# Kernel tuning notes

Measured on AMD Instinct MI355X. Metric: run time of the kernel, lower is better.

The kernel has to match this reference:

```python
import jax, jax.numpy as jnp
import numpy as np


def _diag_perm(h, w):
    # Matches torch loop: offsets -(h-1)..w-1, within offset ordered by row i.
    ii, jj = np.meshgrid(np.arange(h), np.arange(w), indexing='ij')
    idx = np.lexsort((ii.ravel(), (jj - ii).ravel())).astype(np.int32)
    inv = np.argsort(idx).astype(np.int32)
    return jnp.asarray(idx), jnp.asarray(inv)


def _mamba(tok, ln_g, ln_b, Win, conv_w, conv_b, Wx, Wdt, bdt, A_log, Dp, Wout):
    # tok: (B, L, C). MambaLayer = LayerNorm + standard Mamba block.
    di, dc = conv_w.shape
    ds = A_log.shape[-1]
    dtr = Wdt.shape[-1]
    mu = tok.mean(-1, keepdims=True)
    var = ((tok - mu) ** 2).mean(-1, keepdims=True)
    t = (tok - mu) * jax.lax.rsqrt(var + 1e-5) * ln_g + ln_b
    xz = jnp.einsum('blc,ec->ble', t, Win)          # (B,L,2*di)
    xh, z = jnp.split(xz, 2, axis=-1)
    # causal depthwise conv over sequence
    xc = jnp.transpose(xh, (0, 2, 1))               # (B,di,L)
    xc = jax.lax.conv_general_dilated(
        xc, conv_w[:, None, :], (1,), [(dc - 1, 0)],
        dimension_numbers=('NCH', 'OIH', 'NCH'), feature_group_count=di)
    u = jax.nn.silu(jnp.transpose(xc, (0, 2, 1)) + conv_b)  # (B,L,di)
    proj = jnp.einsum('bld,ed->ble', u, Wx)
    dt_r, Bm, Cm = jnp.split(proj, [dtr, dtr + ds], axis=-1)
    dt = jax.nn.softplus(jnp.einsum('blr,dr->bld', dt_r, Wdt) + bdt)  # (B,L,di)
    A = -jnp.exp(A_log)                              # (di,ds)

    def step(h, inp):
        dt_t, B_t, C_t, u_t = inp                    # (B,di) (B,ds) (B,ds) (B,di)
        dA = jnp.exp(dt_t[..., None] * A)            # (B,di,ds)
        h = dA * h + dt_t[..., None] * B_t[:, None, :] * u_t[..., None]
        y = jnp.einsum('bds,bs->bd', h, C_t)
        return h, y

    h0 = jnp.zeros((u.shape[0], di, ds), u.dtype)
    _, ys = jax.lax.scan(step, h0, (jnp.moveaxis(dt, 1, 0), jnp.moveaxis(Bm, 1, 0),
                                    jnp.moveaxis(Cm, 1, 0), jnp.moveaxis(u, 1, 0)))
    y = jnp.moveaxis(ys, 0, 1) + u * Dp              # (B,L,di)
    y = y * jax.nn.silu(z)
    return jnp.einsum('bld,cd->blc', y, Wout)


def _forward(x, ln_g, ln_b, Win, conv_w, conv_b, Wx, Wdt, bdt, A_log, Dp, Wout):
    b, c, h, w = x.shape
    idx, inv = _diag_perm(h, w)

    def mam(d, tok):
        return _mamba(tok, ln_g[d], ln_b[d], Win[d], conv_w[d], conv_b[d],
                      Wx[d], Wdt[d], bdt[d], A_log[d], Dp[d], Wout[d])

    row_tok = x.reshape(b, c, h * w).transpose(0, 2, 1)
    row_feat = mam(0, row_tok).transpose(0, 2, 1).reshape(b, c, h, w)
    col_tok = x.transpose(0, 1, 3, 2).reshape(b, c, w * h).transpose(0, 2, 1)
    col_feat = mam(1, col_tok).transpose(0, 2, 1).reshape(b, c, w, h).transpose(0, 1, 3, 2)
    diag_feat = mam(2, row_tok[:, idx, :])[:, inv, :].transpose(0, 2, 1).reshape(b, c, h, w)
    xf = x[:, :, :, ::-1]
    anti_tok = xf.reshape(b, c, h * w).transpose(0, 2, 1)[:, idx, :]
    anti_feat = mam(3, anti_tok)[:, inv, :].transpose(0, 2, 1).reshape(b, c, h, w)[:, :, :, ::-1]
    gate = jax.nn.sigmoid((row_feat + col_feat + diag_feat + anti_feat) / 4.0)
    return x * gate


def setup_inputs() -> dict:
    key = jax.random.key(0)
    ks = jax.random.split(key, 8)
    B, C, H, W = 4, 96, 48, 48
    DI, DS, DC, DTR = 192, 16, 4, 6
    s = 0.05
    return {
        'x': jax.random.normal(ks[0], (B, C, H, W), jnp.float32),
        'ln_g': jnp.ones((4, C), jnp.float32),
        'ln_b': jnp.zeros((4, C), jnp.float32),
        'Win': jax.random.normal(ks[1], (4, 2 * DI, C), jnp.float32) * s,
        'conv_w': jax.random.normal(ks[2], (4, DI, DC), jnp.float32) * s,
        'conv_b': jnp.zeros((4, DI), jnp.float32),
        'Wx': jax.random.normal(ks[3], (4, DTR + 2 * DS, DI), jnp.float32) * s,
        'Wdt': jax.random.normal(ks[4], (4, DI, DTR), jnp.float32) * s,
        'bdt': jax.random.normal(ks[5], (4, DI), jnp.float32) * s,
        'A_log': jnp.log(jnp.broadcast_to(jnp.arange(1, DS + 1, dtype=jnp.float32), (4, DI, DS))),
        'Dp': jnp.ones((4, DI), jnp.float32),
        'Wout': jax.random.normal(ks[6], (4, C, DI), jnp.float32) * s,
    }


def reference(x, ln_g, ln_b, Win, conv_w, conv_b, Wx, Wdt, bdt, A_log, Dp, Wout):
    return _forward(x, ln_g, ln_b, Win, conv_w, conv_b, Wx, Wdt, bdt, A_log, Dp, Wout)
```

## Files before the change

### kernel.cpp

```cpp
#include <hip/hip_runtime.h>
#include <math.h>

#define LSEQ 2304
#define LC 32
#define NCH 72

typedef unsigned short u16;
typedef unsigned int u32;
typedef __attribute__((ext_vector_type(8))) short bf16x8;
typedef __attribute__((ext_vector_type(4))) float f32x4;

__device__ __forceinline__ float sigmoidf_(float v){ return 1.f/(1.f+__expf(-v)); }
__device__ __forceinline__ u16 f2b(float f){
  union{float f; u32 u;} v; v.f = f;
  u32 r = v.u + 0x7fffu + ((v.u >> 16) & 1u);
  return (u16)(r >> 16);
}
__device__ __forceinline__ float b2f(u16 h){
  union{u32 u; float f;} v; v.u = ((u32)h) << 16; return v.f;
}
__device__ __forceinline__ u16 f2h(float f){
  _Float16 h = (_Float16)f;
  union{_Float16 h; u16 u;} v; v.h = h; return v.u;
}
__device__ __forceinline__ float h2f(u16 u){
  union{u16 u; _Float16 h;} v; v.u = u; return (float)v.h;
}
__device__ __forceinline__ uint2 pack4(float a, float b, float c, float d){
  uint2 o;
  o.x = (u32)f2b(a) | ((u32)f2b(b) << 16);
  o.y = (u32)f2b(c) | ((u32)f2b(d) << 16);
  return o;
}
__device__ __forceinline__ float softplus_(float v){
  return fmaxf(v, 0.f) + __logf(1.f + __expf(-fabsf(v)));
}

__global__ void g_kernel(int* __restrict__ g, int* __restrict__ flag){
  int tid = threadIdx.x;
  if (tid == 0) *flag = 1;
  for (int l = tid; l < LSEQ; l += 256){
    g[l] = l;
    g[LSEQ + l] = (l % 48) * 48 + l / 48;
  }
  for (int p = tid; p < LSEQ; p += 256){
    int i = p / 48, j = p % 48, dd = j - i;
    int off = (dd <= 0) ? (47 + dd) * (48 + dd) / 2
                        : 1176 + 48 * (dd - 1) - dd * (dd - 1) / 2;
    int l = off + min(i, j);
    g[2 * LSEQ + l] = p;
  }
  __syncthreads();
  for (int l = tid; l < LSEQ; l += 256){
    int p2 = g[2 * LSEQ + l];
    g[3 * LSEQ + l] = (p2 / 48) * 48 + 47 - (p2 % 48);
  }
}

__global__ void prep_fold(const float* __restrict__ Win, const float* __restrict__ ln_g,
                          const float* __restrict__ ln_b, const float* __restrict__ A_log,
                          const float* __restrict__ Wout, const float* __restrict__ Wx,
                          const float* __restrict__ Wdt, const float* __restrict__ bdt,
                          u16* __restrict__ WinMF, float* __restrict__ b2,
                          float* __restrict__ Aneg2, u16* __restrict__ WoutMF,
                          u16* __restrict__ Wcomb, float* __restrict__ bcomb,
                          int* __restrict__ flag){
  int i = blockIdx.x * 256 + threadIdx.x;
  if (i < 4*192*16){
    float a = -expf(A_log[i]);
    Aneg2[i] = a * 1.44269504f;
    int s = i & 15;
    float a0 = -expf(A_log[i - s]);
    if (fabsf(a - (float)(s + 1) * a0) > 1e-5f * fabsf(a) + 1e-30f)
      atomicAnd(flag, 0);
  }
  if (i < 4*384*96){
    int d = i / 36864, r = i % 36864, c = r % 96;
    WinMF[i] = f2b(Win[i] * ln_g[d*96 + c]);
  }
  if (i < 4*96*192) WoutMF[i] = f2b(Wout[i]);
  if (i < 4*224*192){
    int d = i / 43008, r = i % 43008, e = r / 192, c = r % 192;
    float w;
    if (e < 192){
      const float* wdt = &Wdt[(size_t)(d*192 + e) * 6];
      w = 0.f;
      #pragma unroll
      for (int r6 = 0; r6 < 6; ++r6) w += wdt[r6] * Wx[(size_t)(d*38 + r6) * 192 + c];
    } else if (e < 208){
      w = Wx[(size_t)(d*38 + 6 + (e - 192)) * 192 + c];
    } else {
      w = Wx[(size_t)(d*38 + 22 + (e - 208)) * 192 + c];
    }
    Wcomb[i] = f2b(w);
  }
  if (i < 4*224){
    int d = i / 224, e = i % 224;
    bcomb[i] = (e < 192) ? bdt[d*192 + e] : 0.f;
  }
  if (i < 4*384){
    int d = i / 384;
    const float* wr = &Win[(size_t)i * 96];
    const float* lb = &ln_b[d * 96];
    float s = 0.f;
    for (int c = 0; c < 96; ++c) s += wr[c] * lb[c];
    b2[i] = s;
  }
}

__global__ __launch_bounds__(256) void ln_kernel(const float* __restrict__ x, u16* __restrict__ n){
  int t = blockIdx.x * 256 + threadIdx.x;
  if (t >= 4 * 2304) return;
  int b = t / 2304, p = t % 2304;
  const float* xp = x + (size_t)b * 96 * 2304 + p;
  float s = 0.f;
  for (int c = 0; c < 96; ++c) s += xp[c * 2304];
  float mu = s * (1.f / 96.f);
  float v = 0.f;
  for (int c = 0; c < 96; ++c){ float dv = xp[c * 2304] - mu; v += dv * dv; }
  float rs = rsqrtf(v * (1.f / 96.f) + 1e-5f);
  u16* np_ = n + (size_t)t * 96;
  for (int c = 0; c < 96; ++c) np_[c] = f2b((xp[c * 2304] - mu) * rs);
}

__global__ __launch_bounds__(256) void kproj(const u16* __restrict__ nbf,
    const u16* __restrict__ WinMF, const float* __restrict__ b2,
    u16* __restrict__ xz){
  int d = blockIdx.y;
  int wv = threadIdx.x >> 6, lane = threadIdx.x & 63;
  int lr = lane & 15, lg = lane >> 4;
  int r0 = blockIdx.x * 64 + wv * 16;
  const u16* Ap = nbf + (size_t)(r0 + lr) * 96 + lg * 8;
  bf16x8 tk0 = *(const bf16x8*)(Ap);
  bf16x8 tk1 = *(const bf16x8*)(Ap + 32);
  bf16x8 tk2 = *(const bf16x8*)(Ap + 64);
  const u16* Wb = WinMF + (size_t)d * 36864 + (size_t)lr * 96 + lg * 8;
  const float* b2d = b2 + d * 384;
  u16* out = xz + ((size_t)d * 9216 + r0 + lr) * 384;
  for (int grp = 0; grp < 3; ++grp){
    f32x4 acc[8];
    #pragma unroll
    for (int t = 0; t < 8; ++t)
      acc[t] = *(const f32x4*)&b2d[(grp*8 + t)*16 + lg*4];
    #pragma unroll
    for (int t = 0; t < 8; ++t){
      const u16* wp = Wb + (size_t)(grp*8 + t) * 1536;
      acc[t] = __builtin_amdgcn_mfma_f32_16x16x32_bf16(*(const bf16x8*)(wp     ), tk0, acc[t], 0, 0, 0);
      acc[t] = __builtin_amdgcn_mfma_f32_16x16x32_bf16(*(const bf16x8*)(wp + 32), tk1, acc[t], 0, 0, 0);
      acc[t] = __builtin_amdgcn_mfma_f32_16x16x32_bf16(*(const bf16x8*)(wp + 64), tk2, acc[t], 0, 0, 0);
    }
    #pragma unroll
    for (int t = 0; t < 8; ++t){
      uint2 o = pack4(acc[t][0], acc[t][1], acc[t][2], acc[t][3]);
      *(uint2*)&out[(grp*8 + t)*16 + lg*4] = o;
    }
  }
}

__global__ __launch_bounds__(256) void kconv(const u16* __restrict__ xz, const int* __restrict__ g,
    const float* __restrict__ conv_w, const float* __restrict__ conv_b,
    u16* __restrict__ u, u16* __restrict__ sz){
  __shared__ u16 xh[67][200];
  int d = blockIdx.z, b = blockIdx.y, l0 = blockIdx.x * 64;
  int tid = threadIdx.x;
  const int* gd = g + d * LSEQ;
  const u16* xzd = xz + (size_t)d * 9216 * 384 + (size_t)b * LSEQ * 384;
  for (int i = tid; i < 67*24; i += 256){
    int lt = i / 24, j = i % 24;
    int gl = l0 - 3 + lt;
    uint4 v = make_uint4(0u, 0u, 0u, 0u);
    if (gl >= 0){
      int p = gd[gl];
      v = *(const uint4*)(xzd + (size_t)p * 384 + j * 8);
    }
    *(uint4*)&xh[lt][j*8] = v;
  }
  size_t obase = ((size_t)(d*4 + b) * LSEQ + l0) * 192;
  for (int i = tid; i < 64*48; i += 256){
    int lt = i / 48, j = (i % 48) * 4;
    int p = gd[l0 + lt];
    uint2 zv = *(const uint2*)(xzd + (size_t)p * 384 + 192 + j);
    float z0 = b2f((u16)(zv.x & 0xffff)), z1 = b2f((u16)(zv.x >> 16));
    float z2 = b2f((u16)(zv.y & 0xffff)), z3 = b2f((u16)(zv.y >> 16));
    z0 *= sigmoidf_(z0); z1 *= sigmoidf_(z1); z2 *= sigmoidf_(z2); z3 *= sigmoidf_(z3);
    *(uint2*)(sz + obase + (size_t)lt * 192 + j) = pack4(z0, z1, z2, z3);
  }
  __syncthreads();
  for (int i = tid; i < 64*48; i += 256){
    int lt = i / 48, j = (i % 48) * 4;
    float a0 = conv_b[d*192 + j + 0];
    float a1 = conv_b[d*192 + j + 1];
    float a2 = conv_b[d*192 + j + 2];
    float a3 = conv_b[d*192 + j + 3];
    const float4 w0 = *(const float4*)&conv_w[(size_t)(d*192 + j + 0) * 4];
    const float4 w1 = *(const float4*)&conv_w[(size_t)(d*192 + j + 1) * 4];
    const float4 w2 = *(const float4*)&conv_w[(size_t)(d*192 + j + 2) * 4];
    const float4 w3 = *(const float4*)&conv_w[(size_t)(d*192 + j + 3) * 4];
    const float* w0p = (const float*)&w0;
    const float* w1p = (const float*)&w1;
    const float* w2p = (const float*)&w2;
    const float* w3p = (const float*)&w3;
    #pragma unroll
    for (int kk = 0; kk < 4; ++kk){
      uint2 xv = *(const uint2*)&xh[lt + kk][j];
      a0 += w0p[kk] * b2f((u16)(xv.x & 0xffff));
      a1 += w1p[kk] * b2f((u16)(xv.x >> 16));
      a2 += w2p[kk] * b2f((u16)(xv.y & 0xffff));
      a3 += w3p[kk] * b2f((u16)(xv.y >> 16));
    }
    a0 *= sigmoidf_(a0); a1 *= sigmoidf_(a1); a2 *= sigmoidf_(a2); a3 *= sigmoidf_(a3);
    *(uint2*)(u + obase + (size_t)lt * 192 + j) = pack4(a0, a1, a2, a3);
  }
}

__global__ __launch_bounds__(256) void kernBM(const u16* __restrict__ u,
    const u16* __restrict__ Wcomb, const float* __restrict__ bcomb,
    u16* __restrict__ dtb, float* __restrict__ Bm, float* __restrict__ Cm){
  __shared__ u16 ush[64 * 200];
  int d = blockIdx.y;
  int tid = threadIdx.x;
  int tile0 = blockIdx.x * 64;
  const u16* ub = u + ((size_t)d * 4 * LSEQ + tile0) * 192;
  for (int i = tid; i < 64*24; i += 256){
    int row = i / 24, c8 = i % 24;
    *(uint4*)&ush[row*200 + c8*8] = *(const uint4*)&ub[(size_t)row*192 + c8*8];
  }
  __syncthreads();
  int wv = tid >> 6, lane = tid & 63;
  int lr = lane & 15, lg = lane >> 4;
  const u16* urow = &ush[(wv*16 + lr)*200 + lg*8];
  bf16x8 tk[6];
  #pragma unroll
  for (int kc = 0; kc < 6; ++kc) tk[kc] = *(const bf16x8*)(urow + kc*32);
  const u16* Wb = Wcomb + (size_t)d * 224 * 192 + (size_t)lr * 192 + lg * 8;
  bf16x8 bw[2][6];
  #pragma unroll
  for (int kc = 0; kc < 6; ++kc) bw[0][kc] = *(const bf16x8*)(Wb + kc*32);
  size_t tokrow = (size_t)d * 4 * LSEQ + tile0 + wv*16 + lr;
  for (int t = 0; t < 14; ++t){
    int cur = t & 1;
    if (t < 13){
      const u16* wp = Wb + (size_t)(t + 1) * 3072;
      #pragma unroll
      for (int kc = 0; kc < 6; ++kc) bw[cur^1][kc] = *(const bf16x8*)(wp + kc*32);
    }
    f32x4 a = (f32x4){0.f, 0.f, 0.f, 0.f};
    #pragma unroll
    for (int kc = 0; kc < 6; ++kc)
      a = __builtin_amdgcn_mfma_f32_16x16x32_bf16(bw[cur][kc], tk[kc], a, 0, 0, 0);
    if (t < 12){
      f32x4 bb = *(const f32x4*)&bcomb[d*224 + t*16 + lg*4];
      float s0 = softplus_(a[0] + bb[0]);
      float s1 = softplus_(a[1] + bb[1]);
      float s2 = softplus_(a[2] + bb[2]);
      float s3 = softplus_(a[3] + bb[3]);
      uint2 o;
      o.x = (u32)f2h(s0) | ((u32)f2h(s1) << 16);
      o.y = (u32)f2h(s2) | ((u32)f2h(s3) << 16);
      *(uint2*)&dtb[tokrow * 192 + t*16 + lg*4] = o;
    } else if (t == 12){
      *(float4*)&Bm[tokrow * 16 + lg*4] = make_float4(a[0], a[1], a[2], a[3]);
    } else {
      *(float4*)&Cm[tokrow * 16 + lg*4] = make_float4(a[0], a[1], a[2], a[3]);
    }
  }
}

__global__ __launch_bounds__(192) void kernC1(const u16* __restrict__ dtb, const u16* __restrict__ u,
    const float* __restrict__ Bm, const float* __restrict__ Aneg2, const int* __restrict__ flag,
    u16* __restrict__ hfin, float* __restrict__ Send){
  __shared__ float Bsh[LC*16];
  int ch = blockIdx.x, b = blockIdx.y, d = blockIdx.z;
  int seq = d*4 + b;
  int di = threadIdx.x;
  size_t tb = (size_t)seq * LSEQ + ch * LC;
  const float* bp = Bm + tb * 16;
  for (int i = di; i < LC*16; i += 192) Bsh[i] = bp[i];
  const u16* dtp = dtb + tb * 192;
  const u16* up  = u   + tb * 192;
  float h[16];
  #pragma unroll
  for (int s = 0; s < 16; ++s) h[s] = 0.f;
  float Sacc = 0.f;
  __syncthreads();
  if (*flag){
    float A2_0 = Aneg2[(d*192 + di) * 16];
    for (int j = 0; j < LC; ++j){
      float dtv = h2f(dtp[j*192 + di]);
      float uv  = b2f(up[j*192 + di]);
      float Bs[16];
      {
        const float4* b4 = (const float4*)&Bsh[j * 16];
        #pragma unroll
        for (int q = 0; q < 4; ++q){ float4 v = b4[q]; Bs[q*4]=v.x; Bs[q*4+1]=v.y; Bs[q*4+2]=v.z; Bs[q*4+3]=v.w; }
      }
      float dtu = dtv * uv;
      float e1 = __builtin_amdgcn_exp2f(dtv * A2_0);
      float e2 = e1*e1, e4 = e2*e2, e8 = e4*e4;
      float p[8];
      p[0]=e1; p[1]=e2; p[2]=e1*e2; p[3]=e4; p[4]=e1*e4; p[5]=e2*e4; p[6]=p[2]*e4; p[7]=e8;
      #pragma unroll
      for (int s = 0; s < 8; ++s){
        h[s] = p[s]*h[s] + dtu*Bs[s];
        float q = p[s]*e8;
        h[s+8] = q*h[s+8] + dtu*Bs[s+8];
      }
      Sacc += dtv;
    }
  } else {
    float A2[16];
    {
      const float4* ap = (const float4*)&Aneg2[(d*192 + di) * 16];
      #pragma unroll
      for (int q = 0; q < 4; ++q){ float4 a4 = ap[q]; A2[q*4]=a4.x; A2[q*4+1]=a4.y; A2[q*4+2]=a4.z; A2[q*4+3]=a4.w; }
    }
    for (int j = 0; j < LC; ++j){
      float dtv = h2f(dtp[j*192 + di]);
      float uv  = b2f(up[j*192 + di]);
      float Bs[16];
      {
        const float4* b4 = (const float4*)&Bsh[j * 16];
        #pragma unroll
        for (int q = 0; q < 4; ++q){ float4 v = b4[q]; Bs[q*4]=v.x; Bs[q*4+1]=v.y; Bs[q*4+2]=v.z; Bs[q*4+3]=v.w; }
      }
      float dtu = dtv * uv;
      #pragma unroll
      for (int s = 0; s < 16; ++s)
        h[s] = __builtin_amdgcn_exp2f(dtv * A2[s]) * h[s] + dtu * Bs[s];
      Sacc += dtv;
    }
  }
  u16* hf = &hfin[((size_t)seq * NCH + ch) * 3072 + di * 16];
  uint4 o0, o1;
  o0.x = (u32)f2b(h[0])  | ((u32)f2b(h[1])  << 16);
  o0.y = (u32)f2b(h[2])  | ((u32)f2b(h[3])  << 16);
  o0.z = (u32)f2b(h[4])  | ((u32)f2b(h[5])  << 16);
  o0.w = (u32)f2b(h[6])  | ((u32)f2b(h[7])  << 16);
  o1.x = (u32)f2b(h[8])  | ((u32)f2b(h[9])  << 16);
  o1.y = (u32)f2b(h[10]) | ((u32)f2b(h[11]) << 16);
  o1.z = (u32)f2b(h[12]) | ((u32)f2b(h[13]) << 16);
  o1.w = (u32)f2b(h[14]) | ((u32)f2b(h[15]) << 16);
  *(uint4*)hf = o0;
  *(uint4*)(hf + 8) = o1;
  Send[((size_t)seq * NCH + ch) * 192 + di] = Sacc;
}

__global__ __launch_bounds__(256) void kernC2(const u16* __restrict__ hfin, const float* __restrict__ Send,
    const float* __restrict__ Aneg2, u16* __restrict__ hin){
  int t = blockIdx.x * 256 + threadIdx.x;
  int seq = t / 3072, q = t % 3072;
  int di = q >> 4, s = q & 15;
  int d = seq >> 2;
  float A2 = Aneg2[(d*192 + di)*16 + s];
  float hr = 0.f;
  const u16* hf = hfin + (size_t)seq * NCH * 3072 + q;
  u16* hi = hin + (size_t)seq * NCH * 3072 + q;
  const float* Se = Send + (size_t)seq * NCH * 192 + di;
  for (int ch = 0; ch < NCH; ++ch){
    hi[(size_t)ch * 3072] = f2b(hr);
    hr = b2f(hf[(size_t)ch * 3072]) + __builtin_amdgcn_exp2f(A2 * Se[(size_t)ch * 192]) * hr;
  }
}

__global__ __launch_bounds__(192) void kernC3(const u16* __restrict__ dtb, const u16* __restrict__ u,
    const float* __restrict__ Bm, const float* __restrict__ Cm,
    const float* __restrict__ Aneg2, const int* __restrict__ flag, const u16* __restrict__ hin,
    const u16* __restrict__ sz, const float* __restrict__ Dp,
    u16* __restrict__ val){
  __shared__ float Bsh[LC*16];
  __shared__ float Csh[LC*16];
  int ch = blockIdx.x, b = blockIdx.y, d = blockIdx.z;
  int seq = d*4 + b;
  int di = threadIdx.x;
  size_t tb = (size_t)seq * LSEQ + ch * LC;
  const float* bp = Bm + tb * 16;
  const float* cp = Cm + tb * 16;
  for (int i = di; i < LC*16; i += 192){ Bsh[i] = bp[i]; Csh[i] = cp[i]; }
  float h[16];
  {
    const uint4* hi4 = (const uint4*)&hin[((size_t)seq * NCH + ch) * 3072 + di * 16];
    uint4 v0 = hi4[0], v1 = hi4[1];
    h[0]=b2f((u16)(v0.x&0xffff)); h[1]=b2f((u16)(v0.x>>16));
    h[2]=b2f((u16)(v0.y&0xffff)); h[3]=b2f((u16)(v0.y>>16));
    h[4]=b2f((u16)(v0.z&0xffff)); h[5]=b2f((u16)(v0.z>>16));
    h[6]=b2f((u16)(v0.w&0xffff)); h[7]=b2f((u16)(v0.w>>16));
    h[8]=b2f((u16)(v1.x&0xffff)); h[9]=b2f((u16)(v1.x>>16));
    h[10]=b2f((u16)(v1.y&0xffff)); h[11]=b2f((u16)(v1.y>>16));
    h[12]=b2f((u16)(v1.z&0xffff)); h[13]=b2f((u16)(v1.z>>16));
    h[14]=b2f((u16)(v1.w&0xffff)); h[15]=b2f((u16)(v1.w>>16));
  }
  float Dpv = Dp[d*192 + di];
  const u16* dtp = dtb + tb * 192;
  const u16* up  = u   + tb * 192;
  const u16* szp = sz  + tb * 192;
  u16* vp = val + tb * 192;
  __syncthreads();
  if (*flag){
    float A2_0 = Aneg2[(d*192 + di) * 16];
    for (int j = 0; j < LC; ++j){
      float dtv = h2f(dtp[j*192 + di]);
      float uv  = b2f(up[j*192 + di]);
      float Bs[16], Cs[16];
      {
        const float4* b4 = (const float4*)&Bsh[j * 16];
        const float4* c4 = (const float4*)&Csh[j * 16];
        #pragma unroll
        for (int q = 0; q < 4; ++q){
          float4 v = b4[q]; Bs[q*4]=v.x; Bs[q*4+1]=v.y; Bs[q*4+2]=v.z; Bs[q*4+3]=v.w;
          float4 w = c4[q]; Cs[q*4]=w.x; Cs[q*4+1]=w.y; Cs[q*4+2]=w.z; Cs[q*4+3]=w.w;
        }
      }
      float dtu = dtv * uv;
      float e1 = __builtin_amdgcn_exp2f(dtv * A2_0);
      float e2 = e1*e1, e4 = e2*e2, e8 = e4*e4;
      float p[8];
      p[0]=e1; p[1]=e2; p[2]=e1*e2; p[3]=e4; p[4]=e1*e4; p[5]=e2*e4; p[6]=p[2]*e4; p[7]=e8;
      float yv = 0.f;
      #pragma unroll
      for (int s = 0; s < 8; ++s){
        h[s] = p[s]*h[s] + dtu*Bs[s];
        yv += h[s]*Cs[s];
        float q = p[s]*e8;
        h[s+8] = q*h[s+8] + dtu*Bs[s+8];
        yv += h[s+8]*Cs[s+8];
      }
      float szv = b2f(szp[j*192 + di]);
      vp[j*192 + di] = f2b((yv + uv * Dpv) * szv);
    }
  } else {
    float A2[16];
    {
      const float4* ap = (const float4*)&Aneg2[(d*192 + di) * 16];
      #pragma unroll
      for (int q = 0; q < 4; ++q){ float4 a4 = ap[q]; A2[q*4]=a4.x; A2[q*4+1]=a4.y; A2[q*4+2]=a4.z; A2[q*4+3]=a4.w; }
    }
    for (int j = 0; j < LC; ++j){
      float dtv = h2f(dtp[j*192 + di]);
      float uv  = b2f(up[j*192 + di]);
      float Bs[16], Cs[16];
      {
        const float4* b4 = (const float4*)&Bsh[j * 16];
        const float4* c4 = (const float4*)&Csh[j * 16];
        #pragma unroll
        for (int q = 0; q < 4; ++q){
          float4 v = b4[q]; Bs[q*4]=v.x; Bs[q*4+1]=v.y; Bs[q*4+2]=v.z; Bs[q*4+3]=v.w;
          float4 w = c4[q]; Cs[q*4]=w.x; Cs[q*4+1]=w.y; Cs[q*4+2]=w.z; Cs[q*4+3]=w.w;
        }
      }
      float dtu = dtv * uv;
      float yv = 0.f;
      #pragma unroll
      for (int s = 0; s < 16; ++s){
        h[s] = __builtin_amdgcn_exp2f(dtv * A2[s]) * h[s] + dtu * Bs[s];
        yv += h[s] * Cs[s];
      }
      float szv = b2f(szp[j*192 + di]);
      vp[j*192 + di] = f2b((yv + uv * Dpv) * szv);
    }
  }
}

__global__ __launch_bounds__(256) void kout(const u16* __restrict__ val,
    const u16* __restrict__ WoutMF, const int* __restrict__ g,
    u16* __restrict__ feat){
  int d = blockIdx.z, b = blockIdx.y;
  int wv = threadIdx.x >> 6, lane = threadIdx.x & 63;
  int lr = lane & 15, lg = lane >> 4;
  int l0 = blockIdx.x * 64 + wv * 16;
  const u16* Ap = val + ((size_t)(d*4 + b) * LSEQ + l0 + lr) * 192 + lg * 8;
  bf16x8 tk[6];
  #pragma unroll
  for (int kc = 0; kc < 6; ++kc) tk[kc] = *(const bf16x8*)(Ap + kc*32);
  const u16* Wb = WoutMF + (size_t)d * 18432 + (size_t)lr * 192 + lg * 8;
  f32x4 acc[6];
  #pragma unroll
  for (int t = 0; t < 6; ++t) acc[t] = (f32x4){0.f, 0.f, 0.f, 0.f};
  #pragma unroll
  for (int t = 0; t < 6; ++t){
    const u16* wp = Wb + (size_t)t * 3072;
    #pragma unroll
    for (int kc = 0; kc < 6; ++kc)
      acc[t] = __builtin_amdgcn_mfma_f32_16x16x32_bf16(*(const bf16x8*)(wp + kc*32), tk[kc], acc[t], 0, 0, 0);
  }
  u16* fd = feat + (size_t)(d*4 + b) * LSEQ * 96;
  int p = g[d*LSEQ + l0 + lr];
  #pragma unroll
  for (int t = 0; t < 6; ++t){
    uint2 o = pack4(acc[t][0], acc[t][1], acc[t][2], acc[t][3]);
    *(uint2*)&fd[(size_t)p * 96 + t*16 + lg*4] = o;
  }
}

__global__ __launch_bounds__(256) void kernE(const float* __restrict__ x, const u16* __restrict__ feat,
    float* __restrict__ out){
  __shared__ float acc[64 * 97];
  int p0 = blockIdx.x * 64, b = blockIdx.y;
  int tid = threadIdx.x;
  const size_t DS_ = (size_t)4 * LSEQ * 96;
  size_t base = ((size_t)b * LSEQ + p0) * 96;
  for (int i = tid; i < 3072; i += 256){
    int pp = i / 48, c2 = (i % 48) * 2;
    size_t o = base + (size_t)pp * 96 + c2;
    u32 v0 = *(const u32*)(feat + o);
    u32 v1 = *(const u32*)(feat + DS_ + o);
    u32 v2 = *(const u32*)(feat + 2*DS_ + o);
    u32 v3 = *(const u32*)(feat + 3*DS_ + o);
    float s0 = b2f((u16)(v0 & 0xffff)) + b2f((u16)(v1 & 0xffff)) + b2f((u16)(v2 & 0xffff)) + b2f((u16)(v3 & 0xffff));
    float s1 = b2f((u16)(v0 >> 16)) + b2f((u16)(v1 >> 16)) + b2f((u16)(v2 >> 16)) + b2f((u16)(v3 >> 16));
    acc[pp*97 + c2] = s0;
    acc[pp*97 + c2 + 1] = s1;
  }
  __syncthreads();
  for (int i = tid; i < 6144; i += 256){
    int c = i / 64, pp = i % 64;
    size_t o = ((size_t)b * 96 + c) * LSEQ + p0 + pp;
    out[o] = x[o] * sigmoidf_(acc[pp*97 + c] * 0.25f);
  }
}

extern "C" void kernel_launch(void* const* d_in, const int* in_sizes, int n_in,
                              void* d_out, int out_size, void* d_ws, size_t ws_size,
                              hipStream_t stream) {
  const float* x      = (const float*)d_in[0];
  const float* ln_g   = (const float*)d_in[1];
  const float* ln_b   = (const float*)d_in[2];
  const float* Win    = (const float*)d_in[3];
  const float* conv_w = (const float*)d_in[4];
  const float* conv_b = (const float*)d_in[5];
  const float* Wx     = (const float*)d_in[6];
  const float* Wdt    = (const float*)d_in[7];
  const float* bdt    = (const float*)d_in[8];
  const float* A_log  = (const float*)d_in[9];
  const float* Dp     = (const float*)d_in[10];
  const float* Wout   = (const float*)d_in[11];

  char* W = (char*)d_ws;
  char* W0 = W;
  auto alloc = [&](size_t bytes) -> char* {
    char* p = W; W += (bytes + 255) & ~(size_t)255; return p;
  };
  int*   g      = (int*)  alloc((size_t)4 * LSEQ * 4);
  int*   flag   = (int*)  alloc(256);
  float* Aneg2  = (float*)alloc((size_t)4 * 192 * 16 * 4);
  float* b2     = (float*)alloc((size_t)4 * 384 * 4);
  u16*   WinMF  = (u16*)  alloc((size_t)4 * 384 * 96 * 2);
  u16*   WoutMF = (u16*)  alloc((size_t)4 * 96 * 192 * 2);
  u16*   Wcomb  = (u16*)  alloc((size_t)4 * 224 * 192 * 2);
  float* bcomb  = (float*)alloc((size_t)4 * 224 * 4);
  u16*   nbf    = (u16*)  alloc((size_t)9216 * 96 * 2);
  u16*   xz     = (u16*)  alloc((size_t)4 * 9216 * 384 * 2);
  u16*   ubf    = (u16*)  alloc((size_t)16 * LSEQ * 192 * 2);
  u16*   szbf   = (u16*)  alloc((size_t)16 * LSEQ * 192 * 2);
  u16*   dtb    = (u16*)  alloc((size_t)16 * LSEQ * 192 * 2);
  float* Bm     = (float*)alloc((size_t)16 * LSEQ * 16 * 4);
  float* Cm     = (float*)alloc((size_t)16 * LSEQ * 16 * 4);
  u16*   valbf  = (u16*)  alloc((size_t)16 * LSEQ * 192 * 2);
  float* Send   = (float*)alloc((size_t)16 * NCH * 192 * 4);
  u16*   hfin   = (u16*)  alloc((size_t)16 * NCH * 3072 * 2);
  u16*   hin    = (u16*)  alloc((size_t)16 * NCH * 3072 * 2);
  u16*   feat   = (u16*)  alloc((size_t)16 * LSEQ * 96 * 2);
  if ((size_t)(W - W0) > ws_size) return;

  g_kernel<<<1, 256, 0, stream>>>(g, flag);
  prep_fold<<<768, 256, 0, stream>>>(Win, ln_g, ln_b, A_log, Wout, Wx, Wdt, bdt,
                                     WinMF, b2, Aneg2, WoutMF, Wcomb, bcomb, flag);
  ln_kernel<<<36, 256, 0, stream>>>(x, nbf);
  kproj<<<dim3(144, 4), 256, 0, stream>>>(nbf, WinMF, b2, xz);
  kconv<<<dim3(36, 4, 4), 256, 0, stream>>>(xz, g, conv_w, conv_b, ubf, szbf);
  kernBM<<<dim3(144, 4), 256, 0, stream>>>(ubf, Wcomb, bcomb, dtb, Bm, Cm);
  kernC1<<<dim3(NCH, 4, 4), 192, 0, stream>>>(dtb, ubf, Bm, Aneg2, flag, hfin, Send);
  kernC2<<<192, 256, 0, stream>>>(hfin, Send, Aneg2, hin);
  kernC3<<<dim3(NCH, 4, 4), 192, 0, stream>>>(dtb, ubf, Bm, Cm, Aneg2, flag, hin, szbf, Dp, valbf);
  kout<<<dim3(36, 4, 4), 256, 0, stream>>>(valbf, WoutMF, g, feat);
  kernE<<<dim3(36, 4), 256, 0, stream>>>(x, feat, (float*)d_out);
}
```

Before: 203.4 us.

## Fuse input projection into conv, scan into out-projection, parallelize LayerNorm

The input projection is now computed inside the conv kernel from gathered normalized tokens staged in shared memory, which removes the large xz intermediate buffer and one launch. The final scan kernel now keeps its outputs in shared memory and applies the Wout MFMA projection directly, which removes the val buffer and the separate kout kernel. LayerNorm splits channels across four threads per position, reduces through shared memory, and writes vectorized stores. The trade-offs are that the projection recomputes 16 halo rows per tile, the fused blocks use more shared memory, and the variance is now computed in one pass as E[x^2]-mu^2.

```diff
diff --git a/kernel.cpp b/kernel.cpp
--- a/kernel.cpp
+++ b/kernel.cpp
@@ -109,83 +109,90 @@
 }
 
 __global__ __launch_bounds__(256) void ln_kernel(const float* __restrict__ x, u16* __restrict__ n){
-  int t = blockIdx.x * 256 + threadIdx.x;
-  if (t >= 4 * 2304) return;
-  int b = t / 2304, p = t % 2304;
+  __shared__ float red[512];
+  int tid = threadIdx.x;
+  int s = tid & 63, q = tid >> 6;
+  int T = blockIdx.x * 64 + s;
+  int b = T / 2304, p = T % 2304;
   const float* xp = x + (size_t)b * 96 * 2304 + p;
-  float s = 0.f;
-  for (int c = 0; c < 96; ++c) s += xp[c * 2304];
-  float mu = s * (1.f / 96.f);
-  float v = 0.f;
-  for (int c = 0; c < 96; ++c){ float dv = xp[c * 2304] - mu; v += dv * dv; }
-  float rs = rsqrtf(v * (1.f / 96.f) + 1e-5f);
-  u16* np_ = n + (size_t)t * 96;
-  for (int c = 0; c < 96; ++c) np_[c] = f2b((xp[c * 2304] - mu) * rs);
-}
-
-__global__ __launch_bounds__(256) void kproj(const u16* __restrict__ nbf,
-    const u16* __restrict__ WinMF, const float* __restrict__ b2,
-    u16* __restrict__ xz){
-  int d = blockIdx.y;
-  int wv = threadIdx.x >> 6, lane = threadIdx.x & 63;
-  int lr = lane & 15, lg = lane >> 4;
-  int r0 = blockIdx.x * 64 + wv * 16;
-  const u16* Ap = nbf + (size_t)(r0 + lr) * 96 + lg * 8;
-  bf16x8 tk0 = *(const bf16x8*)(Ap);
-  bf16x8 tk1 = *(const bf16x8*)(Ap + 32);
-  bf16x8 tk2 = *(const bf16x8*)(Ap + 64);
-  const u16* Wb = WinMF + (size_t)d * 36864 + (size_t)lr * 96 + lg * 8;
-  const float* b2d = b2 + d * 384;
-  u16* out = xz + ((size_t)d * 9216 + r0 + lr) * 384;
-  for (int grp = 0; grp < 3; ++grp){
-    f32x4 acc[8];
-    #pragma unroll
-    for (int t = 0; t < 8; ++t)
-      acc[t] = *(const f32x4*)&b2d[(grp*8 + t)*16 + lg*4];
-    #pragma unroll
-    for (int t = 0; t < 8; ++t){
-      const u16* wp = Wb + (size_t)(grp*8 + t) * 1536;
-      acc[t] = __builtin_amdgcn_mfma_f32_16x16x32_bf16(*(const bf16x8*)(wp     ), tk0, acc[t], 0, 0, 0);
-      acc[t] = __builtin_amdgcn_mfma_f32_16x16x32_bf16(*(const bf16x8*)(wp + 32), tk1, acc[t], 0, 0, 0);
-      acc[t] = __builtin_amdgcn_mfma_f32_16x16x32_bf16(*(const bf16x8*)(wp + 64), tk2, acc[t], 0, 0, 0);
-    }
-    #pragma unroll
-    for (int t = 0; t < 8; ++t){
-      uint2 o = pack4(acc[t][0], acc[t][1], acc[t][2], acc[t][3]);
-      *(uint2*)&out[(grp*8 + t)*16 + lg*4] = o;
-    }
-  }
-}
-
-__global__ __launch_bounds__(256) void kconv(const u16* __restrict__ xz, const int* __restrict__ g,
+  float vals[24];
+  float sum = 0.f, ss = 0.f;
+  #pragma unroll
+  for (int k = 0; k < 24; ++k){
+    float v = xp[(size_t)(q*24 + k) * 2304];
+    vals[k] = v; sum += v; ss += v*v;
+  }
+  red[q*64 + s] = sum;
+  red[256 + q*64 + s] = ss;
+  __syncthreads();
+  float S = red[s] + red[64+s] + red[128+s] + red[192+s];
+  float Q = red[256+s] + red[320+s] + red[384+s] + red[448+s];
+  float mu = S * (1.f/96.f);
+  float var = Q * (1.f/96.f) - mu*mu;
+  float rs = rsqrtf(var + 1e-5f);
+  u32 w[12];
+  #pragma unroll
+  for (int k = 0; k < 12; ++k){
+    float v0 = (vals[2*k]   - mu) * rs;
+    float v1 = (vals[2*k+1] - mu) * rs;
+    w[k] = (u32)f2b(v0) | ((u32)f2b(v1) << 16);
+  }
+  uint4* np_ = (uint4*)(n + (size_t)T * 96 + q*24);
+  np_[0] = make_uint4(w[0], w[1], w[2],  w[3]);
+  np_[1] = make_uint4(w[4], w[5], w[6],  w[7]);
+  np_[2] = make_uint4(w[8], w[9], w[10], w[11]);
+}
+
+__global__ __launch_bounds__(256) void kprojconv(const u16* __restrict__ nbf,
+    const int* __restrict__ g, const u16* __restrict__ WinMF, const float* __restrict__ b2,
     const float* __restrict__ conv_w, const float* __restrict__ conv_b,
     u16* __restrict__ u, u16* __restrict__ sz){
-  __shared__ u16 xh[67][200];
+  __shared__ u16 tl[80][200];
+  __shared__ u16 xh[80][200];
   int d = blockIdx.z, b = blockIdx.y, l0 = blockIdx.x * 64;
   int tid = threadIdx.x;
+  int seq = d*4 + b;
   const int* gd = g + d * LSEQ;
-  const u16* xzd = xz + (size_t)d * 9216 * 384 + (size_t)b * LSEQ * 384;
-  for (int i = tid; i < 67*24; i += 256){
-    int lt = i / 24, j = i % 24;
+  for (int i = tid; i < 67*12; i += 256){
+    int lt = i / 12, j = i % 12;
     int gl = l0 - 3 + lt;
     uint4 v = make_uint4(0u, 0u, 0u, 0u);
     if (gl >= 0){
       int p = gd[gl];
-      v = *(const uint4*)(xzd + (size_t)p * 384 + j * 8);
-    }
-    *(uint4*)&xh[lt][j*8] = v;
-  }
-  size_t obase = ((size_t)(d*4 + b) * LSEQ + l0) * 192;
-  for (int i = tid; i < 64*48; i += 256){
-    int lt = i / 48, j = (i % 48) * 4;
-    int p = gd[l0 + lt];
-    uint2 zv = *(const uint2*)(xzd + (size_t)p * 384 + 192 + j);
-    float z0 = b2f((u16)(zv.x & 0xffff)), z1 = b2f((u16)(zv.x >> 16));
-    float z2 = b2f((u16)(zv.y & 0xffff)), z3 = b2f((u16)(zv.y >> 16));
-    z0 *= sigmoidf_(z0); z1 *= sigmoidf_(z1); z2 *= sigmoidf_(z2); z3 *= sigmoidf_(z3);
-    *(uint2*)(sz + obase + (size_t)lt * 192 + j) = pack4(z0, z1, z2, z3);
-  }
-  __syncthreads();
+      v = *(const uint4*)(nbf + (size_t)(b*2304 + p) * 96 + j*8);
+    }
+    *(uint4*)&tl[lt][j*8] = v;
+  }
+  __syncthreads();
+  int wv = tid >> 6, lane = tid & 63;
+  int lr = lane & 15, lg = lane >> 4;
+  const u16* Wb = WinMF + (size_t)d * 36864 + (size_t)lr * 96 + lg * 8;
+  const float* b2d = b2 + d * 384;
+  size_t zbase = (size_t)seq * LSEQ * 192;
+  for (int rt = wv; rt < 5; rt += 4){
+    int row = rt*16 + lr;
+    bf16x8 tk0 = *(const bf16x8*)&tl[row][      lg*8];
+    bf16x8 tk1 = *(const bf16x8*)&tl[row][32  + lg*8];
+    bf16x8 tk2 = *(const bf16x8*)&tl[row][64  + lg*8];
+    bool valid = (l0 + row >= 3);
+    for (int te = 0; te < 24; ++te){
+      const u16* wp = Wb + (size_t)te * 1536;
+      f32x4 acc = *(const f32x4*)&b2d[te*16 + lg*4];
+      acc = __builtin_amdgcn_mfma_f32_16x16x32_bf16(*(const bf16x8*)(wp     ), tk0, acc, 0, 0, 0);
+      acc = __builtin_amdgcn_mfma_f32_16x16x32_bf16(*(const bf16x8*)(wp + 32), tk1, acc, 0, 0, 0);
+      acc = __builtin_amdgcn_mfma_f32_16x16x32_bf16(*(const bf16x8*)(wp + 64), tk2, acc, 0, 0, 0);
+      if (te < 12){
+        uint2 o = valid ? pack4(acc[0], acc[1], acc[2], acc[3]) : make_uint2(0u, 0u);
+        *(uint2*)&xh[row][te*16 + lg*4] = o;
+      } else if (row >= 3 && row < 67){
+        float z0 = acc[0], z1 = acc[1], z2 = acc[2], z3 = acc[3];
+        z0 *= sigmoidf_(z0); z1 *= sigmoidf_(z1); z2 *= sigmoidf_(z2); z3 *= sigmoidf_(z3);
+        *(uint2*)(sz + zbase + (size_t)(l0 + row - 3) * 192 + (te-12)*16 + lg*4) = pack4(z0, z1, z2, z3);
+      }
+    }
+  }
+  __syncthreads();
+  size_t obase = ((size_t)seq * LSEQ + l0) * 192;
   for (int i = tid; i < 64*48; i += 256){
     int lt = i / 48, j = (i % 48) * 4;
     float a0 = conv_b[d*192 + j + 0];
@@ -362,20 +369,26 @@
   }
 }
 
-__global__ __launch_bounds__(192) void kernC3(const u16* __restrict__ dtb, const u16* __restrict__ u,
+__global__ __launch_bounds__(384) void kscan2out(const u16* __restrict__ dtb, const u16* __restrict__ u,
     const float* __restrict__ Bm, const float* __restrict__ Cm,
     const float* __restrict__ Aneg2, const int* __restrict__ flag, const u16* __restrict__ hin,
     const u16* __restrict__ sz, const float* __restrict__ Dp,
-    u16* __restrict__ val){
-  __shared__ float Bsh[LC*16];
-  __shared__ float Csh[LC*16];
-  int ch = blockIdx.x, b = blockIdx.y, d = blockIdx.z;
+    const u16* __restrict__ WoutMF, const int* __restrict__ g,
+    u16* __restrict__ feat){
+  __shared__ float Bsh[64*16];
+  __shared__ float Csh[64*16];
+  __shared__ u16 vsh[64][200];
+  int b = blockIdx.y, d = blockIdx.z;
   int seq = d*4 + b;
-  int di = threadIdx.x;
-  size_t tb = (size_t)seq * LSEQ + ch * LC;
-  const float* bp = Bm + tb * 16;
-  const float* cp = Cm + tb * 16;
-  for (int i = di; i < LC*16; i += 192){ Bsh[i] = bp[i]; Csh[i] = cp[i]; }
+  int l0 = blockIdx.x * 64;
+  int tid = threadIdx.x;
+  int gc = tid / 192, di = tid % 192;
+  int ch = blockIdx.x * 2 + gc;
+  {
+    const float* bp = Bm + ((size_t)seq * LSEQ + l0) * 16;
+    const float* cp = Cm + ((size_t)seq * LSEQ + l0) * 16;
+    for (int i = tid; i < 64*16; i += 384){ Bsh[i] = bp[i]; Csh[i] = cp[i]; }
+  }
   float h[16];
   {
     const uint4* hi4 = (const uint4*)&hin[((size_t)seq * NCH + ch) * 3072 + di * 16];
@@ -390,10 +403,10 @@
     h[14]=b2f((u16)(v1.w&0xffff)); h[15]=b2f((u16)(v1.w>>16));
   }
   float Dpv = Dp[d*192 + di];
+  size_t tb = (size_t)seq * LSEQ + ch * LC;
   const u16* dtp = dtb + tb * 192;
   const u16* up  = u   + tb * 192;
   const u16* szp = sz  + tb * 192;
-  u16* vp = val + tb * 192;
   __syncthreads();
   if (*flag){
     float A2_0 = Aneg2[(d*192 + di) * 16];
@@ -402,8 +415,8 @@
       float uv  = b2f(up[j*192 + di]);
       float Bs[16], Cs[16];
       {
-        const float4* b4 = (const float4*)&Bsh[j * 16];
-        const float4* c4 = (const float4*)&Csh[j * 16];
+        const float4* b4 = (const float4*)&Bsh[(gc*32 + j) * 16];
+        const float4* c4 = (const float4*)&Csh[(gc*32 + j) * 16];
         #pragma unroll
         for (int q = 0; q < 4; ++q){
           float4 v = b4[q]; Bs[q*4]=v.x; Bs[q*4+1]=v.y; Bs[q*4+2]=v.z; Bs[q*4+3]=v.w;
@@ -425,7 +438,7 @@
         yv += h[s+8]*Cs[s+8];
       }
       float szv = b2f(szp[j*192 + di]);
-      vp[j*192 + di] = f2b((yv + uv * Dpv) * szv);
+      vsh[gc*32 + j][di] = f2b((yv + uv * Dpv) * szv);
     }
   } else {
     float A2[16];
@@ -439,8 +452,8 @@
       float uv  = b2f(up[j*192 + di]);
       float Bs[16], Cs[16];
       {
-        const float4* b4 = (const float4*)&Bsh[j * 16];
-        const float4* c4 = (const float4*)&Csh[j * 16];
+        const float4* b4 = (const float4*)&Bsh[(gc*32 + j) * 16];
+        const float4* c4 = (const float4*)&Csh[(gc*32 + j) * 16];
         #pragma unroll
         for (int q = 0; q < 4; ++q){
           float4 v = b4[q]; Bs[q*4]=v.x; Bs[q*4+1]=v.y; Bs[q*4+2]=v.z; Bs[q*4+3]=v.w;
@@ -455,39 +468,35 @@
         yv += h[s] * Cs[s];
       }
       float szv = b2f(szp[j*192 + di]);
-      vp[j*192 + di] = f2b((yv + uv * Dpv) * szv);
-    }
-  }
-}
-
-__global__ __launch_bounds__(256) void kout(const u16* __restrict__ val,
-    const u16* __restrict__ WoutMF, const int* __restrict__ g,
-    u16* __restrict__ feat){
-  int d = blockIdx.z, b = blockIdx.y;
-  int wv = threadIdx.x >> 6, lane = threadIdx.x & 63;
-  int lr = lane & 15, lg = lane >> 4;
-  int l0 = blockIdx.x * 64 + wv * 16;
-  const u16* Ap = val + ((size_t)(d*4 + b) * LSEQ + l0 + lr) * 192 + lg * 8;
-  bf16x8 tk[6];
-  #pragma unroll
-  for (int kc = 0; kc < 6; ++kc) tk[kc] = *(const bf16x8*)(Ap + kc*32);
-  const u16* Wb = WoutMF + (size_t)d * 18432 + (size_t)lr * 192 + lg * 8;
-  f32x4 acc[6];
-  #pragma unroll
-  for (int t = 0; t < 6; ++t) acc[t] = (f32x4){0.f, 0.f, 0.f, 0.f};
-  #pragma unroll
-  for (int t = 0; t < 6; ++t){
-    const u16* wp = Wb + (size_t)t * 3072;
+      vsh[gc*32 + j][di] = f2b((yv + uv * Dpv) * szv);
+    }
+  }
+  __syncthreads();
+  if (tid < 256){
+    int wv = tid >> 6, lane = tid & 63;
+    int lr = lane & 15, lg = lane >> 4;
+    bf16x8 tk[6];
     #pragma unroll
     for (int kc = 0; kc < 6; ++kc)
-      acc[t] = __builtin_amdgcn_mfma_f32_16x16x32_bf16(*(const bf16x8*)(wp + kc*32), tk[kc], acc[t], 0, 0, 0);
-  }
-  u16* fd = feat + (size_t)(d*4 + b) * LSEQ * 96;
-  int p = g[d*LSEQ + l0 + lr];
-  #pragma unroll
-  for (int t = 0; t < 6; ++t){
-    uint2 o = pack4(acc[t][0], acc[t][1], acc[t][2], acc[t][3]);
-    *(uint2*)&fd[(size_t)p * 96 + t*16 + lg*4] = o;
+      tk[kc] = *(const bf16x8*)&vsh[wv*16 + lr][kc*32 + lg*8];
+    const u16* Wb = WoutMF + (size_t)d * 18432 + (size_t)lr * 192 + lg * 8;
+    f32x4 acc[6];
+    #pragma unroll
+    for (int t = 0; t < 6; ++t) acc[t] = (f32x4){0.f, 0.f, 0.f, 0.f};
+    #pragma unroll
+    for (int t = 0; t < 6; ++t){
+      const u16* wp = Wb + (size_t)t * 3072;
+      #pragma unroll
+      for (int kc = 0; kc < 6; ++kc)
+        acc[t] = __builtin_amdgcn_mfma_f32_16x16x32_bf16(*(const bf16x8*)(wp + kc*32), tk[kc], acc[t], 0, 0, 0);
+    }
+    u16* fd = feat + (size_t)seq * LSEQ * 96;
+    int p = g[d*LSEQ + l0 + wv*16 + lr];
+    #pragma unroll
+    for (int t = 0; t < 6; ++t){
+      uint2 o = pack4(acc[t][0], acc[t][1], acc[t][2], acc[t][3]);
+      *(uint2*)&fd[(size_t)p * 96 + t*16 + lg*4] = o;
+    }
   }
 }
 
@@ -548,13 +557,11 @@
   u16*   Wcomb  = (u16*)  alloc((size_t)4 * 224 * 192 * 2);
   float* bcomb  = (float*)alloc((size_t)4 * 224 * 4);
   u16*   nbf    = (u16*)  alloc((size_t)9216 * 96 * 2);
-  u16*   xz     = (u16*)  alloc((size_t)4 * 9216 * 384 * 2);
   u16*   ubf    = (u16*)  alloc((size_t)16 * LSEQ * 192 * 2);
   u16*   szbf   = (u16*)  alloc((size_t)16 * LSEQ * 192 * 2);
   u16*   dtb    = (u16*)  alloc((size_t)16 * LSEQ * 192 * 2);
   float* Bm     = (float*)alloc((size_t)16 * LSEQ * 16 * 4);
   float* Cm     = (float*)alloc((size_t)16 * LSEQ * 16 * 4);
-  u16*   valbf  = (u16*)  alloc((size_t)16 * LSEQ * 192 * 2);
   float* Send   = (float*)alloc((size_t)16 * NCH * 192 * 4);
   u16*   hfin   = (u16*)  alloc((size_t)16 * NCH * 3072 * 2);
   u16*   hin    = (u16*)  alloc((size_t)16 * NCH * 3072 * 2);
@@ -564,13 +571,12 @@
   g_kernel<<<1, 256, 0, stream>>>(g, flag);
   prep_fold<<<768, 256, 0, stream>>>(Win, ln_g, ln_b, A_log, Wout, Wx, Wdt, bdt,
                                      WinMF, b2, Aneg2, WoutMF, Wcomb, bcomb, flag);
-  ln_kernel<<<36, 256, 0, stream>>>(x, nbf);
-  kproj<<<dim3(144, 4), 256, 0, stream>>>(nbf, WinMF, b2, xz);
-  kconv<<<dim3(36, 4, 4), 256, 0, stream>>>(xz, g, conv_w, conv_b, ubf, szbf);
+  ln_kernel<<<144, 256, 0, stream>>>(x, nbf);
+  kprojconv<<<dim3(36, 4, 4), 256, 0, stream>>>(nbf, g, WinMF, b2, conv_w, conv_b, ubf, szbf);
   kernBM<<<dim3(144, 4), 256, 0, stream>>>(ubf, Wcomb, bcomb, dtb, Bm, Cm);
   kernC1<<<dim3(NCH, 4, 4), 192, 0, stream>>>(dtb, ubf, Bm, Aneg2, flag, hfin, Send);
   kernC2<<<192, 256, 0, stream>>>(hfin, Send, Aneg2, hin);
-  kernC3<<<dim3(NCH, 4, 4), 192, 0, stream>>>(dtb, ubf, Bm, Cm, Aneg2, flag, hin, szbf, Dp, valbf);
-  kout<<<dim3(36, 4, 4), 256, 0, stream>>>(valbf, WoutMF, g, feat);
+  kscan2out<<<dim3(36, 4, 4), 384, 0, stream>>>(dtb, ubf, Bm, Cm, Aneg2, flag, hin, szbf, Dp,
+                                                WoutMF, g, feat);
   kernE<<<dim3(36, 4), 256, 0, stream>>>(x, feat, (float*)d_out);
 }
```

Measured after the change: 206.8 us. About the same (+1.7%).
